# Kernel optimization log

Hardware: AMD Instinct MI355X
Metric: run time of the kernel (lower is better)

## Reference

```python
import jax, jax.numpy as jnp
import numpy as np

B, T, J, D = 128, 256, 50, 3
I, H, C = J * D, 1024, 60


def setup_inputs() -> dict:
    key = jax.random.key(0)
    ks = jax.random.split(key, 10)
    s = 0.02
    return {
        "x": jax.random.normal(ks[0], (B, T, J, D), dtype=jnp.float32),
        "h1": jnp.zeros((B, H), jnp.float32),
        "c1": jnp.zeros((B, H), jnp.float32),
        "h2": jnp.zeros((B, H), jnp.float32),
        "c2": jnp.zeros((B, H), jnp.float32),
        "W_ih1": jax.random.normal(ks[1], (4 * H, I), jnp.float32) * s,
        "W_hh1": jax.random.normal(ks[2], (4 * H, H), jnp.float32) * s,
        "b_ih1": jax.random.normal(ks[3], (4 * H,), jnp.float32) * s,
        "b_hh1": jax.random.normal(ks[4], (4 * H,), jnp.float32) * s,
        "W_ih2": jax.random.normal(ks[5], (4 * H, H), jnp.float32) * s,
        "W_hh2": jax.random.normal(ks[6], (4 * H, H), jnp.float32) * s,
        "b_ih2": jax.random.normal(ks[7], (4 * H,), jnp.float32) * s,
        "b_hh2": jax.random.normal(ks[8], (4 * H,), jnp.float32) * s,
        "W_fc": jax.random.normal(ks[9], (C, H), jnp.float32) * s,
        "b_fc": jnp.zeros((C,), jnp.float32),
        "mode": 0,  # 0 == 'val' (no dropout), static
    }


def _lstm_cell(xv, h, c, Wih, Whh, bih, bhh):
    # PyTorch LSTMCell gate order: i, f, g, o
    gates = xv @ Wih.T + bih + h @ Whh.T + bhh  # [B, 4H]
    i, f, g, o = jnp.split(gates, 4, axis=-1)
    c_new = jax.nn.sigmoid(f) * c + jax.nn.sigmoid(i) * jnp.tanh(g)
    h_new = jax.nn.sigmoid(o) * jnp.tanh(c_new)
    return h_new, c_new


def reference(x, h1, c1, h2, c2, W_ih1, W_hh1, b_ih1, b_hh1,
              W_ih2, W_hh2, b_ih2, b_hh2, W_fc, b_fc, mode):
    b, t = x.shape[0], x.shape[1]
    xs = x.reshape(b, t, -1).transpose(1, 0, 2)  # [T, B, I]

    def step(carry, xt):
        h1, c1, h2, c2 = carry
        h1, c1 = _lstm_cell(xt, h1, c1, W_ih1, W_hh1, b_ih1, b_hh1)
        # mode==0 ('val'): no dropout between layers
        h2, c2 = _lstm_cell(h1, h2, c2, W_ih2, W_hh2, b_ih2, b_hh2)
        return (h1, c1, h2, c2), None

    (h1, c1, h2, c2), _ = jax.lax.scan(step, (h1, c1, h2, c2), xs)
    return h2 @ W_fc.T + b_fc  # [B, num_class]
```

## Files before the change

kernel.cpp:

```cpp
#include <hip/hip_runtime.h>
#include <math.h>


typedef __bf16 bf16;
typedef __bf16 bf16x8 __attribute__((ext_vector_type(8)));
typedef float floatx4 __attribute__((ext_vector_type(4)));
typedef unsigned long long ull;

#define B_   128
#define T_   256
#define H_   1024
#define I_   150
#define KX_  160
#define C_   60
#define K1LDS 1280
#define KP    1024
#define NLINES 40
#define CSTRIDE 64
#define L0FLAG 32
#define L1FLAG 33
#define NCOLS 32
#define NHC  8
#define NT   2

template<int N> struct IC { static constexpr int value = N; };

__device__ __forceinline__ float sigmoidf_(float x) { return 1.f / (1.f + expf(-x)); }

__global__ __launch_bounds__(256)
void convert_all(const float* __restrict__ x,
                 const float* __restrict__ h1in, const float* __restrict__ h2in,
                 bf16* __restrict__ xb, bf16* __restrict__ h1b0, bf16* __restrict__ h2b0,
                 unsigned* __restrict__ cnt)
{
    const size_t nXB = (size_t)T_ * B_ * KX_;
    const size_t nHC = (size_t)B_ * H_;
    size_t idx = (size_t)blockIdx.x * 256 + threadIdx.x;

    if (idx < nXB) {
        size_t t = idx / (B_ * KX_);
        size_t r = idx - t * (B_ * KX_);
        size_t b = r / KX_, k = r - b * KX_;
        xb[idx] = (k < I_) ? (bf16)x[(b * T_ + t) * I_ + k] : (bf16)0.f;
        return;
    }
    idx -= nXB;
    if (idx < nHC) { h1b0[idx] = (bf16)h1in[idx]; return; }
    idx -= nHC;
    if (idx < nHC) { h2b0[idx] = (bf16)h2in[idx]; return; }
    idx -= nHC;
    if (idx < NLINES * CSTRIDE) cnt[idx] = 0u;
}

__device__ __forceinline__ void stage_rebal(
    bf16* lds, bf16* ldsP, int tid, int layer, int n0h,
    const float* Wih1, const float* Whh1, const float* Wih2, const float* Whh2)
{
    if (layer == 0) {
        {
            const int cpr = K1LDS >> 3;
            const int total = NCOLS * cpr;
            for (int ci = tid; ci < total; ci += 512) {
                int r = ci / cpr, c = ci - r * cpr;
                int g = r / NHC, j = r - g * NHC;
                int grow = (g << 10) + n0h + j;
                int k0 = c << 3;
                float v[8];
#pragma unroll
                for (int u = 0; u < 8; ++u) {
                    int k = k0 + u;
                    v[u] = (k < I_) ? Wih1[(size_t)grow * I_ + k]
                         : (k < KX_) ? 0.f
                         : (k < KX_ + H_) ? Whh1[(size_t)grow * H_ + (k - KX_)] : 0.f;
                }
                int cs = (c & ~15) | ((c ^ r) & 15);
                bf16* dst = lds + (size_t)r * K1LDS + (cs << 3);
#pragma unroll
                for (int u = 0; u < 8; ++u) dst[u] = (bf16)v[u];
            }
        }
        {
            const int cpr = KP >> 3;
            const int total = NCOLS * cpr;
            for (int ci = tid; ci < total; ci += 512) {
                int r = ci / cpr, c = ci - r * cpr;
                int g = r / NHC, j = r - g * NHC;
                int grow = (g << 10) + n0h + j;
                int k0 = c << 3;
                float v[8];
#pragma unroll
                for (int u = 0; u < 8; ++u) v[u] = Wih2[(size_t)grow * H_ + k0 + u];
                int cs = (c & ~15) | ((c ^ r) & 15);
                bf16* dst = ldsP + (size_t)r * KP + (cs << 3);
#pragma unroll
                for (int u = 0; u < 8; ++u) dst[u] = (bf16)v[u];
            }
        }
    } else {
        const int cpr = KP >> 3;
        const int total = NCOLS * cpr;
        for (int ci = tid; ci < total; ci += 512) {
            int r = ci / cpr, c = ci - r * cpr;
            int g = r / NHC, j = r - g * NHC;
            int grow = (g << 10) + n0h + j;
            int k0 = c << 3;
            float v[8];
#pragma unroll
            for (int u = 0; u < 8; ++u) v[u] = Whh2[(size_t)grow * H_ + k0 + u];
            int cs = (c & ~15) | ((c ^ r) & 15);
            bf16* dst = lds + (size_t)r * KP + (cs << 3);
#pragma unroll
            for (int u = 0; u < 8; ++u) dst[u] = (bf16)v[u];
        }
    }
}

__global__ __launch_bounds__(512, 2)
void rnn_dist8(const bf16* __restrict__ xb,
               bf16* __restrict__ h1b0, bf16* __restrict__ h1b1,
               bf16* __restrict__ h2b0, bf16* __restrict__ h2b1,
               float* __restrict__ p0, float* __restrict__ p1, float* __restrict__ p2,
               const float* __restrict__ c1in, const float* __restrict__ c2in,
               const float* __restrict__ Wih1, const float* __restrict__ Whh1,
               const float* __restrict__ bih1, const float* __restrict__ bhh1,
               const float* __restrict__ Wih2, const float* __restrict__ Whh2,
               const float* __restrict__ bih2, const float* __restrict__ bhh2,
               const float* __restrict__ Wfc, const float* __restrict__ bfc,
               float* __restrict__ out, unsigned* __restrict__ cnt, int nblk)
{
    extern __shared__ bf16 lds[];
    __shared__ __align__(16) bf16 hst[8][16][NHC];

    const int tid   = threadIdx.x;
    const int bid   = blockIdx.x;
    const int layer = (bid >> 3) & 1;
    const int slice = (bid & 7) | ((bid >> 4) << 3);
    const int n0h   = slice * NHC;
    const int line  = layer * 16 + ((bid & 7) | (((bid >> 4) & 1) << 3));
    bf16* ldsP = lds + 32 * K1LDS;

    stage_rebal(lds, ldsP, tid, layer, n0h, Wih1, Whh1, Wih2, Whh2);
    __syncthreads();

    const int lane = tid & 63;
    const int wv   = tid >> 6;
    const int jj   = lane & (NHC - 1);
    const int quad = lane >> 4;

    float4 bias;
    {
        const float* bi = layer ? bih2 : bih1;
        const float* bh = layer ? bhh2 : bhh1;
        int col = n0h + jj;
        bias.x = bi[col] + bh[col];
        bias.y = bi[col + H_] + bh[col + H_];
        bias.z = bi[col + 2 * H_] + bh[col + 2 * H_];
        bias.w = bi[col + 3 * H_] + bh[col + 3 * H_];
    }

    float creg[2];
    {
        const float* cin = layer ? c2in : c1in;
        int dup = (lane >> 3) & 1;
#pragma unroll
        for (int rp = 0; rp < 2; ++rp) {
            int row = wv * 16 + quad * 4 + rp * 2 + dup;
            creg[rp] = cin[(size_t)row * H_ + n0h + jj];
        }
    }

    floatx4 acc[NT];
    floatx4 pacc[NT];

    auto seg1 = [&](const bf16* A, int ldA, const bf16* Bb, int ldB,
                    auto nksC, int ksBase) {
        constexpr int NKS = decltype(nksC)::value;
        constexpr int CH  = NKS < 16 ? NKS : 16;
        const int arow = wv * 16 + (lane & 15);
        const bf16* a0 = A + (size_t)arow * ldA + quad * 8;
        for (int blk = 0; blk < NKS; blk += CH) {
            bf16x8 a0r[CH];
#pragma unroll
            for (int i = 0; i < CH; ++i)
                a0r[i] = *(const bf16x8*)(a0 + (blk + i) * 32);
            __builtin_amdgcn_sched_barrier(0);
#pragma unroll
            for (int i = 0; i < CH; ++i) {
                int c = (ksBase + blk + i) * 4 + quad;
#pragma unroll
                for (int t = 0; t < NT; ++t) {
                    int r = t * 16 + (lane & 15);
                    int cs = (c & ~15) | ((c ^ r) & 15);
                    bf16x8 bfr = *(const bf16x8*)(Bb + (size_t)r * ldB + (cs << 3));
                    acc[t] = __builtin_amdgcn_mfma_f32_16x16x32_bf16(a0r[i], bfr, acc[t], 0, 0, 0);
                }
            }
        }
    };

    auto segDual = [&](const bf16* A) {
        const int arow = wv * 16 + (lane & 15);
        const bf16* a0 = A + (size_t)arow * H_ + quad * 8;
        for (int blk = 0; blk < 32; blk += 16) {
            bf16x8 a0r[16];
#pragma unroll
            for (int i = 0; i < 16; ++i)
                a0r[i] = *(const bf16x8*)(a0 + (blk + i) * 32);
            __builtin_amdgcn_sched_barrier(0);
#pragma unroll
            for (int i = 0; i < 16; ++i) {
                int ig = blk + i;
                int c1 = (5 + ig) * 4 + quad;
                int cp = ig * 4 + quad;
#pragma unroll
                for (int t = 0; t < NT; ++t) {
                    int r = t * 16 + (lane & 15);
                    int cs1 = (c1 & ~15) | ((c1 ^ r) & 15);
                    bf16x8 b1 = *(const bf16x8*)(lds + (size_t)r * K1LDS + (cs1 << 3));
                    acc[t] = __builtin_amdgcn_mfma_f32_16x16x32_bf16(a0r[i], b1, acc[t], 0, 0, 0);
                    int csp = (cp & ~15) | ((cp ^ r) & 15);
                    bf16x8 bp = *(const bf16x8*)(ldsP + (size_t)r * KP + (csp << 3));
                    pacc[t] = __builtin_amdgcn_mfma_f32_16x16x32_bf16(a0r[i], bp, pacc[t], 0, 0, 0);
                }
            }
        }
    };

    auto epilogue = [&](bf16* hw) {
        const int base = lane & 48;
#pragma unroll
        for (int r = 0; r < 4; ++r) {
            float vi = __shfl(acc[0][r], base + jj, 64);
            float vf = __shfl(acc[0][r], base + 8 + jj, 64);
            float vg = __shfl(acc[1][r], base + jj, 64);
            float vo = __shfl(acc[1][r], base + 8 + jj, 64);
            bool cond = (((lane >> 3) & 1) == (r & 1));
            int slot = r >> 1;
            if (cond) {
                float cv = creg[slot];
                float cn = sigmoidf_(vf + bias.y) * cv
                         + sigmoidf_(vi + bias.x) * tanhf(vg + bias.z);
                creg[slot] = cn;
                float hn = sigmoidf_(vo + bias.w) * tanhf(cn);
                hst[wv][quad * 4 + r][jj] = (bf16)hn;
            }
        }
        __syncthreads();
        if (lane < 32) {
            int row_l = lane >> 1, cg = lane & 1;
            ull v = *(const ull*)&hst[wv][row_l][cg * 4];
            __hip_atomic_store((ull*)(hw + (size_t)(wv * 16 + row_l) * H_ + n0h + cg * 4),
                               v, __ATOMIC_RELAXED, __HIP_MEMORY_SCOPE_AGENT);
        }
    };

    if (layer == 0) {
#pragma unroll
        for (int t = 0; t < NT; ++t) {
            acc[t]  = (floatx4){0.f, 0.f, 0.f, 0.f};
            pacc[t] = (floatx4){0.f, 0.f, 0.f, 0.f};
        }
        seg1(xb, KX_, lds, K1LDS, IC<5>{}, 0);
    }

    for (int e = 0; e <= T_ + 1; ++e) {
        const int pm  = e % 3;
        const int pmr = (e + 2) % 3;
        float* const pbuf[3] = { p0, p1, p2 };

        if (layer == 0 && e <= T_) {
            const bf16* h1r = (e & 1) ? h1b1 : h1b0;
            segDual(h1r);

            float* pw = pbuf[pm] + (size_t)slice * B_ * NCOLS;
#pragma unroll
            for (int t = 0; t < NT; ++t)
#pragma unroll
                for (int r = 0; r < 4; ++r) {
                    int row = wv * 16 + quad * 4 + r;
                    __hip_atomic_store(pw + (size_t)row * NCOLS + t * 16 + (lane & 15),
                                       pacc[t][r], __ATOMIC_RELAXED, __HIP_MEMORY_SCOPE_AGENT);
                }

            if (e < T_) {
                bf16* hw = (e & 1) ? h1b0 : h1b1;
                epilogue(hw);
            }
        } else if (layer == 1 && e >= 2) {
#pragma unroll
            for (int t = 0; t < NT; ++t) acc[t] = (floatx4){0.f, 0.f, 0.f, 0.f};

            const float* pr = pbuf[pmr] + (size_t)slice * B_ * NCOLS;
            float pv[NT][4];
#pragma unroll
            for (int t = 0; t < NT; ++t)
#pragma unroll
                for (int r = 0; r < 4; ++r) {
                    int row = wv * 16 + quad * 4 + r;
                    pv[t][r] = pr[(size_t)row * NCOLS + t * 16 + (lane & 15)];
                }

            const bf16* h2r = (e & 1) ? h2b1 : h2b0;
            seg1(h2r, H_, lds, KP, IC<32>{}, 0);

#pragma unroll
            for (int t = 0; t < NT; ++t)
#pragma unroll
                for (int r = 0; r < 4; ++r) acc[t][r] += pv[t][r];

            bf16* hw = (e & 1) ? h2b0 : h2b1;
            epilogue(hw);
        }

        asm volatile("s_waitcnt vmcnt(0)" ::: "memory");
        __syncthreads();
        const int etag = e + 1;
        if (tid == 0)
            __hip_atomic_fetch_add(cnt + line * CSTRIDE, 1u,
                                   __ATOMIC_RELAXED, __HIP_MEMORY_SCOPE_AGENT);
        if (layer == 0 && e < T_) {
#pragma unroll
            for (int t = 0; t < NT; ++t) {
                acc[t]  = (floatx4){0.f, 0.f, 0.f, 0.f};
                pacc[t] = (floatx4){0.f, 0.f, 0.f, 0.f};
            }
            if (e + 1 < T_)
                seg1(xb + (size_t)(e + 1) * B_ * KX_, KX_, lds, K1LDS, IC<5>{}, 0);
        }
        if (tid < 64) {
            const unsigned* cp = nullptr;
            unsigned tgt = 0;
            if (lane < 16) {
                cp = cnt + (layer * 16 + lane) * CSTRIDE;
                tgt = 8u * (unsigned)etag;
            } else if (lane < 32) {
                if (layer == 0) {
                    if (etag >= 3) {
                        cp = cnt + (16 + (lane - 16)) * CSTRIDE;
                        tgt = 8u * (unsigned)(etag - 2);
                    }
                } else {
                    cp = cnt + (lane - 16) * CSTRIDE;
                    tgt = 8u * (unsigned)etag;
                }
            }
            for (;;) {
                bool ok = (cp == nullptr) ||
                          (__hip_atomic_load(cp, __ATOMIC_RELAXED,
                                             __HIP_MEMORY_SCOPE_AGENT) >= tgt);
                if (__all(ok)) break;
                __builtin_amdgcn_s_sleep(1);
            }
            __builtin_amdgcn_fence(__ATOMIC_ACQUIRE, "agent");
        }
        __syncthreads();
    }

    if (tid < 64) {
        if (lane < 16) {
            const unsigned* cp = cnt + (16 + lane) * CSTRIDE;
            while (__hip_atomic_load(cp, __ATOMIC_RELAXED,
                                     __HIP_MEMORY_SCOPE_AGENT) < 8u * (unsigned)(T_ + 2))
                __builtin_amdgcn_s_sleep(1);
        }
        __builtin_amdgcn_fence(__ATOMIC_ACQUIRE, "agent");
    }
    __syncthreads();

    if (bid < B_) {
        const bf16* h2f = h2b0;
        for (int c = wv; c < C_; c += 8) {
            float a = 0.f;
            for (int k = lane; k < H_; k += 64)
                a += (float)h2f[(size_t)bid * H_ + k] * Wfc[(size_t)c * H_ + k];
#pragma unroll
            for (int off = 32; off; off >>= 1) a += __shfl_down(a, off, 64);
            if (lane == 0) out[bid * C_ + c] = a + bfc[c];
        }
    }
}

__global__ __launch_bounds__(512, 2)
void rnn_decoup8(const bf16* __restrict__ xb,
                 bf16* __restrict__ h1b0, bf16* __restrict__ h1b1,
                 bf16* __restrict__ h2b0, bf16* __restrict__ h2b1,
                 float* __restrict__ p0, float* __restrict__ p1, float* __restrict__ p2,
                 const float* __restrict__ c1in, const float* __restrict__ c2in,
                 const float* __restrict__ Wih1, const float* __restrict__ Whh1,
                 const float* __restrict__ bih1, const float* __restrict__ bhh1,
                 const float* __restrict__ Wih2, const float* __restrict__ Whh2,
                 const float* __restrict__ bih2, const float* __restrict__ bhh2,
                 const float* __restrict__ Wfc, const float* __restrict__ bfc,
                 float* __restrict__ out, unsigned* __restrict__ cnt, int nblk)
{
    extern __shared__ bf16 lds[];
    __shared__ __align__(16) bf16 hst[8][16][NHC];

    const int tid   = threadIdx.x;
    const int bid   = blockIdx.x;
    const int layer = (bid >> 3) & 1;
    const int slice = (bid & 7) | ((bid >> 4) << 3);
    const int n0h   = slice * NHC;
    const int line  = layer * 16 + ((bid & 7) | (((bid >> 4) & 1) << 3));
    bf16* ldsP = lds + 32 * K1LDS;

    stage_rebal(lds, ldsP, tid, layer, n0h, Wih1, Whh1, Wih2, Whh2);
    __syncthreads();

    const int lane = tid & 63;
    const int wv   = tid >> 6;
    const int jj   = lane & (NHC - 1);
    const int quad = lane >> 4;

    float4 bias;
    {
        const float* bi = layer ? bih2 : bih1;
        const float* bh = layer ? bhh2 : bhh1;
        int col = n0h + jj;
        bias.x = bi[col] + bh[col];
        bias.y = bi[col + H_] + bh[col + H_];
        bias.z = bi[col + 2 * H_] + bh[col + 2 * H_];
        bias.w = bi[col + 3 * H_] + bh[col + 3 * H_];
    }

    float creg[2];
    {
        const float* cin = layer ? c2in : c1in;
        int dup = (lane >> 3) & 1;
#pragma unroll
        for (int rp = 0; rp < 2; ++rp) {
            int row = wv * 16 + quad * 4 + rp * 2 + dup;
            creg[rp] = cin[(size_t)row * H_ + n0h + jj];
        }
    }

    floatx4 acc[NT];
    floatx4 pacc[NT];

    auto seg1 = [&](const bf16* A, int ldA, const bf16* Bb, int ldB,
                    auto nksC, int ksBase) {
        constexpr int NKS = decltype(nksC)::value;
        constexpr int CH  = NKS < 16 ? NKS : 16;
        const int arow = wv * 16 + (lane & 15);
        const bf16* a0 = A + (size_t)arow * ldA + quad * 8;
        for (int blk = 0; blk < NKS; blk += CH) {
            bf16x8 a0r[CH];
#pragma unroll
            for (int i = 0; i < CH; ++i)
                a0r[i] = *(const bf16x8*)(a0 + (blk + i) * 32);
            __builtin_amdgcn_sched_barrier(0);
#pragma unroll
            for (int i = 0; i < CH; ++i) {
                int c = (ksBase + blk + i) * 4 + quad;
#pragma unroll
                for (int t = 0; t < NT; ++t) {
                    int r = t * 16 + (lane & 15);
                    int cs = (c & ~15) | ((c ^ r) & 15);
                    bf16x8 bfr = *(const bf16x8*)(Bb + (size_t)r * ldB + (cs << 3));
                    acc[t] = __builtin_amdgcn_mfma_f32_16x16x32_bf16(a0r[i], bfr, acc[t], 0, 0, 0);
                }
            }
        }
    };

    auto segDual = [&](const bf16* A) {
        const int arow = wv * 16 + (lane & 15);
        const bf16* a0 = A + (size_t)arow * H_ + quad * 8;
        for (int blk = 0; blk < 32; blk += 16) {
            bf16x8 a0r[16];
#pragma unroll
            for (int i = 0; i < 16; ++i)
                a0r[i] = *(const bf16x8*)(a0 + (blk + i) * 32);
            __builtin_amdgcn_sched_barrier(0);
#pragma unroll
            for (int i = 0; i < 16; ++i) {
                int ig = blk + i;
                int c1 = (5 + ig) * 4 + quad;
                int cp = ig * 4 + quad;
#pragma unroll
                for (int t = 0; t < NT; ++t) {
                    int r = t * 16 + (lane & 15);
                    int cs1 = (c1 & ~15) | ((c1 ^ r) & 15);
                    bf16x8 b1 = *(const bf16x8*)(lds + (size_t)r * K1LDS + (cs1 << 3));
                    acc[t] = __builtin_amdgcn_mfma_f32_16x16x32_bf16(a0r[i], b1, acc[t], 0, 0, 0);
                    int csp = (cp & ~15) | ((cp ^ r) & 15);
                    bf16x8 bp = *(const bf16x8*)(ldsP + (size_t)r * KP + (csp << 3));
                    pacc[t] = __builtin_amdgcn_mfma_f32_16x16x32_bf16(a0r[i], bp, pacc[t], 0, 0, 0);
                }
            }
        }
    };

    auto epilogue = [&](bf16* hw) {
        const int base = lane & 48;
#pragma unroll
        for (int r = 0; r < 4; ++r) {
            float vi = __shfl(acc[0][r], base + jj, 64);
            float vf = __shfl(acc[0][r], base + 8 + jj, 64);
            float vg = __shfl(acc[1][r], base + jj, 64);
            float vo = __shfl(acc[1][r], base + 8 + jj, 64);
            bool cond = (((lane >> 3) & 1) == (r & 1));
            int slot = r >> 1;
            if (cond) {
                float cv = creg[slot];
                float cn = sigmoidf_(vf + bias.y) * cv
                         + sigmoidf_(vi + bias.x) * tanhf(vg + bias.z);
                creg[slot] = cn;
                float hn = sigmoidf_(vo + bias.w) * tanhf(cn);
                hst[wv][quad * 4 + r][jj] = (bf16)hn;
            }
        }
        __syncthreads();
        if (lane < 32) {
            int row_l = lane >> 1, cg = lane & 1;
            ull v = *(const ull*)&hst[wv][row_l][cg * 4];
            __hip_atomic_store((ull*)(hw + (size_t)(wv * 16 + row_l) * H_ + n0h + cg * 4),
                               v, __ATOMIC_RELAXED, __HIP_MEMORY_SCOPE_AGENT);
        }
    };

    if (layer == 0) {
#pragma unroll
        for (int t = 0; t < NT; ++t) {
            acc[t]  = (floatx4){0.f, 0.f, 0.f, 0.f};
            pacc[t] = (floatx4){0.f, 0.f, 0.f, 0.f};
        }
        seg1(xb, KX_, lds, K1LDS, IC<5>{}, 0);
    }

    for (int e = 0; e <= T_ + 1; ++e) {
        const int pm  = e % 3;
        const int pmr = (e + 2) % 3;
        float* const pbuf[3] = { p0, p1, p2 };

        if (layer == 0 && e <= T_) {
            const bf16* h1r = (e & 1) ? h1b1 : h1b0;
            segDual(h1r);

            float* pw = pbuf[pm] + (size_t)slice * B_ * NCOLS;
#pragma unroll
            for (int t = 0; t < NT; ++t)
#pragma unroll
                for (int r = 0; r < 4; ++r) {
                    int row = wv * 16 + quad * 4 + r;
                    __hip_atomic_store(pw + (size_t)row * NCOLS + t * 16 + (lane & 15),
                                       pacc[t][r], __ATOMIC_RELAXED, __HIP_MEMORY_SCOPE_AGENT);
                }

            if (e < T_) {
                bf16* hw = (e & 1) ? h1b0 : h1b1;
                epilogue(hw);
            }
        } else if (layer == 1 && e >= 2) {
#pragma unroll
            for (int t = 0; t < NT; ++t) acc[t] = (floatx4){0.f, 0.f, 0.f, 0.f};

            const float* pr = pbuf[pmr] + (size_t)slice * B_ * NCOLS;
            float pv[NT][4];
#pragma unroll
            for (int t = 0; t < NT; ++t)
#pragma unroll
                for (int r = 0; r < 4; ++r) {
                    int row = wv * 16 + quad * 4 + r;
                    pv[t][r] = pr[(size_t)row * NCOLS + t * 16 + (lane & 15)];
                }

            const bf16* h2r = (e & 1) ? h2b1 : h2b0;
            seg1(h2r, H_, lds, KP, IC<32>{}, 0);

#pragma unroll
            for (int t = 0; t < NT; ++t)
#pragma unroll
                for (int r = 0; r < 4; ++r) acc[t][r] += pv[t][r];

            bf16* hw = (e & 1) ? h2b0 : h2b1;
            epilogue(hw);
        }

        asm volatile("s_waitcnt vmcnt(0)" ::: "memory");
        __syncthreads();
        const int etag = e + 1;
        if (tid == 0)
            __hip_atomic_fetch_add(cnt + line * CSTRIDE, 1u,
                                   __ATOMIC_RELAXED, __HIP_MEMORY_SCOPE_AGENT);
        if (layer == 0 && e < T_) {
#pragma unroll
            for (int t = 0; t < NT; ++t) {
                acc[t]  = (floatx4){0.f, 0.f, 0.f, 0.f};
                pacc[t] = (floatx4){0.f, 0.f, 0.f, 0.f};
            }
            if (e + 1 < T_)
                seg1(xb + (size_t)(e + 1) * B_ * KX_, KX_, lds, K1LDS, IC<5>{}, 0);
        }
        if (layer == 0) {
            if (bid == 0) {
                if (tid < 16) {
                    const unsigned tgt = 8u * (unsigned)etag;
                    const unsigned* cp = cnt + tid * CSTRIDE;
                    while (__hip_atomic_load(cp, __ATOMIC_RELAXED, __HIP_MEMORY_SCOPE_AGENT) < tgt)
                        __builtin_amdgcn_s_sleep(1);
                }
                if (tid == 0)
                    __hip_atomic_store(cnt + L0FLAG * CSTRIDE, (unsigned)etag,
                                       __ATOMIC_RELAXED, __HIP_MEMORY_SCOPE_AGENT);
            } else if (tid == 0) {
                const unsigned* fp = cnt + L0FLAG * CSTRIDE;
                while (__hip_atomic_load(fp, __ATOMIC_RELAXED, __HIP_MEMORY_SCOPE_AGENT) < (unsigned)etag)
                    __builtin_amdgcn_s_sleep(1);
            }
            if (tid == 0 && etag >= 3) {
                const unsigned* fp = cnt + L1FLAG * CSTRIDE;
                while (__hip_atomic_load(fp, __ATOMIC_RELAXED, __HIP_MEMORY_SCOPE_AGENT) < (unsigned)(etag - 2))
                    __builtin_amdgcn_s_sleep(1);
            }
        } else {
            if (bid == 8) {
                if (tid < 16) {
                    const unsigned tgt = 8u * (unsigned)etag;
                    const unsigned* cp = cnt + (16 + tid) * CSTRIDE;
                    while (__hip_atomic_load(cp, __ATOMIC_RELAXED, __HIP_MEMORY_SCOPE_AGENT) < tgt)
                        __builtin_amdgcn_s_sleep(1);
                }
                if (tid == 0)
                    __hip_atomic_store(cnt + L1FLAG * CSTRIDE, (unsigned)etag,
                                       __ATOMIC_RELAXED, __HIP_MEMORY_SCOPE_AGENT);
            } else if (tid == 0) {
                const unsigned* fp = cnt + L1FLAG * CSTRIDE;
                while (__hip_atomic_load(fp, __ATOMIC_RELAXED, __HIP_MEMORY_SCOPE_AGENT) < (unsigned)etag)
                    __builtin_amdgcn_s_sleep(1);
            }
            if (tid == 0) {
                const unsigned* fp = cnt + L0FLAG * CSTRIDE;
                while (__hip_atomic_load(fp, __ATOMIC_RELAXED, __HIP_MEMORY_SCOPE_AGENT) < (unsigned)etag)
                    __builtin_amdgcn_s_sleep(1);
            }
        }
        __syncthreads();
        if (tid < 64)
            __builtin_amdgcn_fence(__ATOMIC_ACQUIRE, "agent");
        __syncthreads();
    }

    if (tid == 0 && layer == 0) {
        const unsigned* fp = cnt + L1FLAG * CSTRIDE;
        while (__hip_atomic_load(fp, __ATOMIC_RELAXED, __HIP_MEMORY_SCOPE_AGENT) < (unsigned)(T_ + 2))
            __builtin_amdgcn_s_sleep(1);
    }
    __syncthreads();
    if (tid < 64)
        __builtin_amdgcn_fence(__ATOMIC_ACQUIRE, "agent");
    __syncthreads();

    if (bid < B_) {
        const bf16* h2f = h2b0;
        for (int c = wv; c < C_; c += 8) {
            float a = 0.f;
            for (int k = lane; k < H_; k += 64)
                a += (float)h2f[(size_t)bid * H_ + k] * Wfc[(size_t)c * H_ + k];
#pragma unroll
            for (int off = 32; off; off >>= 1) a += __shfl_down(a, off, 64);
            if (lane == 0) out[bid * C_ + c] = a + bfc[c];
        }
    }
}

extern "C" void kernel_launch(void* const* d_in, const int* in_sizes, int n_in,
                              void* d_out, int out_size, void* d_ws, size_t ws_size,
                              hipStream_t stream)
{
    const float* x    = (const float*)d_in[0];
    const float* h1in = (const float*)d_in[1];
    const float* c1in = (const float*)d_in[2];
    const float* h2in = (const float*)d_in[3];
    const float* c2in = (const float*)d_in[4];
    const float* Wih1 = (const float*)d_in[5];
    const float* Whh1 = (const float*)d_in[6];
    const float* bih1 = (const float*)d_in[7];
    const float* bhh1 = (const float*)d_in[8];
    const float* Wih2 = (const float*)d_in[9];
    const float* Whh2 = (const float*)d_in[10];
    const float* bih2 = (const float*)d_in[11];
    const float* bhh2 = (const float*)d_in[12];
    const float* Wfc  = (const float*)d_in[13];
    const float* bfc  = (const float*)d_in[14];
    float* out = (float*)d_out;

    const size_t szXB  = (size_t)T_ * B_ * KX_ * 2;
    const size_t szH   = (size_t)B_ * H_ * 2;
    const size_t szCnt = (size_t)NLINES * CSTRIDE * 4;
    const size_t szP   = (size_t)128 * B_ * NCOLS * 4;
    const size_t needDec = szXB + 4 * szH + szCnt + 3 * szP;

    char* p = (char*)d_ws;
    bf16* xb = (bf16*)p;    p += szXB;
    bf16* h1b0 = (bf16*)p;  p += szH;
    bf16* h1b1 = (bf16*)p;  p += szH;
    bf16* h2b0 = (bf16*)p;  p += szH;
    bf16* h2b1 = (bf16*)p;  p += szH;
    unsigned* cnt = (unsigned*)p;  p += szCnt;
    float* p0 = (float*)p;  p += szP;
    float* p1 = (float*)p;  p += szP;
    float* p2 = (float*)p;

    const size_t citems = (size_t)T_ * B_ * KX_ + 2 * (size_t)B_ * H_ + NLINES * CSTRIDE;
    convert_all<<<(int)((citems + 255) / 256), 256, 0, stream>>>(
        x, h1in, h2in, xb, h1b0, h2b0, cnt);

    int nblk = 256;
    void* args[] = { &xb, &h1b0, &h1b1, &h2b0, &h2b1, &p0, &p1, &p2,
                     (void*)&c1in, (void*)&c2in,
                     (void*)&Wih1, (void*)&Whh1, (void*)&bih1, (void*)&bhh1,
                     (void*)&Wih2, (void*)&Whh2, (void*)&bih2, (void*)&bhh2,
                     (void*)&Wfc, (void*)&bfc, &out, &cnt, &nblk };

    const unsigned ldsRebal = (unsigned)(32 * K1LDS + 32 * KP) * 2u;
    hipError_t err = hipErrorOutOfMemory;
    if (ws_size >= needDec) {
        if (hipFuncSetAttribute((const void*)rnn_dist8,
                                hipFuncAttributeMaxDynamicSharedMemorySize,
                                (int)ldsRebal) == hipSuccess) {
            err = hipLaunchCooperativeKernel((const void*)rnn_dist8,
                                             dim3(256), dim3(512), args,
                                             ldsRebal, stream);
        }
    }
    if (err != hipSuccess && ws_size >= needDec) {
        (void)hipGetLastError();
        if (hipFuncSetAttribute((const void*)rnn_decoup8,
                                hipFuncAttributeMaxDynamicSharedMemorySize,
                                (int)ldsRebal) == hipSuccess) {
            (void)hipLaunchCooperativeKernel((const void*)rnn_decoup8,
                                             dim3(256), dim3(512), args,
                                             ldsRebal, stream);
        }
    }
}
```

Measured before the change: 3.329 ms.

## Pack cross-layer partials to bf16, use fast activations, centralize barrier flags

The layer-0 to layer-1 input-projection partials are stored as packed bf16 pairs instead of fp32, halving that per-step exchange traffic. Sigmoid and tanh switch to fast exp and reciprocal approximations. The per-step inter-block barrier changes from every block polling 16-32 line counters to one leader block per layer polling the counters and publishing a single flag that the other blocks wait on. This removes polling contention but adds an extra hop of latency per step, and the bf16 partials and approximate activations cost precision.

```diff
diff --git a/kernel.cpp b/kernel.cpp
--- a/kernel.cpp
+++ b/kernel.cpp
@@ -27,6 +27,15 @@
 
 __device__ __forceinline__ float sigmoidf_(float x) { return 1.f / (1.f + expf(-x)); }
 
+__device__ __forceinline__ float fsig(float x) {
+    return __builtin_amdgcn_rcpf(1.f + __expf(-x));
+}
+__device__ __forceinline__ float ftanh(float x) {
+    float t = __expf(-2.f * fabsf(x));
+    float r = (1.f - t) * __builtin_amdgcn_rcpf(1.f + t);
+    return copysignf(r, x);
+}
+
 __global__ __launch_bounds__(256)
 void convert_all(const float* __restrict__ x,
                  const float* __restrict__ h1in, const float* __restrict__ h2in,
@@ -116,17 +125,17 @@
 }
 
 __global__ __launch_bounds__(512, 2)
-void rnn_dist8(const bf16* __restrict__ xb,
-               bf16* __restrict__ h1b0, bf16* __restrict__ h1b1,
-               bf16* __restrict__ h2b0, bf16* __restrict__ h2b1,
-               float* __restrict__ p0, float* __restrict__ p1, float* __restrict__ p2,
-               const float* __restrict__ c1in, const float* __restrict__ c2in,
-               const float* __restrict__ Wih1, const float* __restrict__ Whh1,
-               const float* __restrict__ bih1, const float* __restrict__ bhh1,
-               const float* __restrict__ Wih2, const float* __restrict__ Whh2,
-               const float* __restrict__ bih2, const float* __restrict__ bhh2,
-               const float* __restrict__ Wfc, const float* __restrict__ bfc,
-               float* __restrict__ out, unsigned* __restrict__ cnt, int nblk)
+void rnn_bf16p8(const bf16* __restrict__ xb,
+                bf16* __restrict__ h1b0, bf16* __restrict__ h1b1,
+                bf16* __restrict__ h2b0, bf16* __restrict__ h2b1,
+                float* __restrict__ p0, float* __restrict__ p1, float* __restrict__ p2,
+                const float* __restrict__ c1in, const float* __restrict__ c2in,
+                const float* __restrict__ Wih1, const float* __restrict__ Whh1,
+                const float* __restrict__ bih1, const float* __restrict__ bhh1,
+                const float* __restrict__ Wih2, const float* __restrict__ Whh2,
+                const float* __restrict__ bih2, const float* __restrict__ bhh2,
+                const float* __restrict__ Wfc, const float* __restrict__ bfc,
+                float* __restrict__ out, unsigned* __restrict__ cnt, int nblk)
 {
     extern __shared__ bf16 lds[];
     __shared__ __align__(16) bf16 hst[8][16][NHC];
@@ -238,10 +247,10 @@
             int slot = r >> 1;
             if (cond) {
                 float cv = creg[slot];
-                float cn = sigmoidf_(vf + bias.y) * cv
-                         + sigmoidf_(vi + bias.x) * tanhf(vg + bias.z);
+                float cn = fsig(vf + bias.y) * cv
+                         + fsig(vi + bias.x) * ftanh(vg + bias.z);
                 creg[slot] = cn;
-                float hn = sigmoidf_(vo + bias.w) * tanhf(cn);
+                float hn = fsig(vo + bias.w) * ftanh(cn);
                 hst[wv][quad * 4 + r][jj] = (bf16)hn;
             }
         }
@@ -272,15 +281,17 @@
             const bf16* h1r = (e & 1) ? h1b1 : h1b0;
             segDual(h1r);
 
-            float* pw = pbuf[pm] + (size_t)slice * B_ * NCOLS;
-#pragma unroll
-            for (int t = 0; t < NT; ++t)
-#pragma unroll
-                for (int r = 0; r < 4; ++r) {
-                    int row = wv * 16 + quad * 4 + r;
-                    __hip_atomic_store(pw + (size_t)row * NCOLS + t * 16 + (lane & 15),
-                                       pacc[t][r], __ATOMIC_RELAXED, __HIP_MEMORY_SCOPE_AGENT);
-                }
+            unsigned* pw = (unsigned*)pbuf[pm] + (size_t)slice * B_ * 16;
+#pragma unroll
+            for (int r = 0; r < 4; ++r) {
+                int row = wv * 16 + quad * 4 + r;
+                bf16 b0 = (bf16)pacc[0][r];
+                bf16 b1 = (bf16)pacc[1][r];
+                unsigned u = (unsigned)(*(unsigned short*)&b0)
+                           | ((unsigned)(*(unsigned short*)&b1) << 16);
+                __hip_atomic_store(pw + (size_t)row * 16 + (lane & 15), u,
+                                   __ATOMIC_RELAXED, __HIP_MEMORY_SCOPE_AGENT);
+            }
 
             if (e < T_) {
                 bf16* hw = (e & 1) ? h1b0 : h1b1;
@@ -290,15 +301,17 @@
 #pragma unroll
             for (int t = 0; t < NT; ++t) acc[t] = (floatx4){0.f, 0.f, 0.f, 0.f};
 
-            const float* pr = pbuf[pmr] + (size_t)slice * B_ * NCOLS;
+            const unsigned* pr = (const unsigned*)pbuf[pmr] + (size_t)slice * B_ * 16;
             float pv[NT][4];
 #pragma unroll
-            for (int t = 0; t < NT; ++t)
-#pragma unroll
-                for (int r = 0; r < 4; ++r) {
-                    int row = wv * 16 + quad * 4 + r;
-                    pv[t][r] = pr[(size_t)row * NCOLS + t * 16 + (lane & 15)];
-                }
+            for (int r = 0; r < 4; ++r) {
+                int row = wv * 16 + quad * 4 + r;
+                unsigned u = pr[(size_t)row * 16 + (lane & 15)];
+                unsigned short s0 = (unsigned short)(u & 0xffffu);
+                unsigned short s1 = (unsigned short)(u >> 16);
+                pv[0][r] = (float)(*(bf16*)&s0);
+                pv[1][r] = (float)(*(bf16*)&s1);
+            }
 
             const bf16* h2r = (e & 1) ? h2b1 : h2b0;
             seg1(h2r, H_, lds, KP, IC<32>{}, 0);
@@ -327,44 +340,63 @@
             if (e + 1 < T_)
                 seg1(xb + (size_t)(e + 1) * B_ * KX_, KX_, lds, K1LDS, IC<5>{}, 0);
         }
-        if (tid < 64) {
-            const unsigned* cp = nullptr;
-            unsigned tgt = 0;
-            if (lane < 16) {
-                cp = cnt + (layer * 16 + lane) * CSTRIDE;
-                tgt = 8u * (unsigned)etag;
-            } else if (lane < 32) {
-                if (layer == 0) {
-                    if (etag >= 3) {
-                        cp = cnt + (16 + (lane - 16)) * CSTRIDE;
-                        tgt = 8u * (unsigned)(etag - 2);
-                    }
-                } else {
-                    cp = cnt + (lane - 16) * CSTRIDE;
-                    tgt = 8u * (unsigned)etag;
-                }
-            }
-            for (;;) {
-                bool ok = (cp == nullptr) ||
-                          (__hip_atomic_load(cp, __ATOMIC_RELAXED,
-                                             __HIP_MEMORY_SCOPE_AGENT) >= tgt);
-                if (__all(ok)) break;
-                __builtin_amdgcn_s_sleep(1);
-            }
+        if (layer == 0) {
+            if (bid == 0) {
+                if (tid < 16) {
+                    const unsigned tgt = 8u * (unsigned)etag;
+                    const unsigned* cp = cnt + tid * CSTRIDE;
+                    while (__hip_atomic_load(cp, __ATOMIC_RELAXED, __HIP_MEMORY_SCOPE_AGENT) < tgt)
+                        __builtin_amdgcn_s_sleep(1);
+                }
+                if (tid == 0)
+                    __hip_atomic_store(cnt + L0FLAG * CSTRIDE, (unsigned)etag,
+                                       __ATOMIC_RELAXED, __HIP_MEMORY_SCOPE_AGENT);
+            } else if (tid == 0) {
+                const unsigned* fp = cnt + L0FLAG * CSTRIDE;
+                while (__hip_atomic_load(fp, __ATOMIC_RELAXED, __HIP_MEMORY_SCOPE_AGENT) < (unsigned)etag)
+                    __builtin_amdgcn_s_sleep(1);
+            }
+            if (tid == 0 && etag >= 3) {
+                const unsigned* fp = cnt + L1FLAG * CSTRIDE;
+                while (__hip_atomic_load(fp, __ATOMIC_RELAXED, __HIP_MEMORY_SCOPE_AGENT) < (unsigned)(etag - 2))
+                    __builtin_amdgcn_s_sleep(1);
+            }
+        } else {
+            if (bid == 8) {
+                if (tid < 16) {
+                    const unsigned tgt = 8u * (unsigned)etag;
+                    const unsigned* cp = cnt + (16 + tid) * CSTRIDE;
+                    while (__hip_atomic_load(cp, __ATOMIC_RELAXED, __HIP_MEMORY_SCOPE_AGENT) < tgt)
+                        __builtin_amdgcn_s_sleep(1);
+                }
+                if (tid == 0)
+                    __hip_atomic_store(cnt + L1FLAG * CSTRIDE, (unsigned)etag,
+                                       __ATOMIC_RELAXED, __HIP_MEMORY_SCOPE_AGENT);
+            } else if (tid == 0) {
+                const unsigned* fp = cnt + L1FLAG * CSTRIDE;
+                while (__hip_atomic_load(fp, __ATOMIC_RELAXED, __HIP_MEMORY_SCOPE_AGENT) < (unsigned)etag)
+                    __builtin_amdgcn_s_sleep(1);
+            }
+            if (tid == 0) {
+                const unsigned* fp = cnt + L0FLAG * CSTRIDE;
+                while (__hip_atomic_load(fp, __ATOMIC_RELAXED, __HIP_MEMORY_SCOPE_AGENT) < (unsigned)etag)
+                    __builtin_amdgcn_s_sleep(1);
+            }
+        }
+        __syncthreads();
+        if (tid < 64)
             __builtin_amdgcn_fence(__ATOMIC_ACQUIRE, "agent");
-        }
         __syncthreads();
     }
 
-    if (tid < 64) {
-        if (lane < 16) {
-            const unsigned* cp = cnt + (16 + lane) * CSTRIDE;
-            while (__hip_atomic_load(cp, __ATOMIC_RELAXED,
-                                     __HIP_MEMORY_SCOPE_AGENT) < 8u * (unsigned)(T_ + 2))
-                __builtin_amdgcn_s_sleep(1);
-        }
+    if (tid == 0 && layer == 0) {
+        const unsigned* fp = cnt + L1FLAG * CSTRIDE;
+        while (__hip_atomic_load(fp, __ATOMIC_RELAXED, __HIP_MEMORY_SCOPE_AGENT) < (unsigned)(T_ + 2))
+            __builtin_amdgcn_s_sleep(1);
+    }
+    __syncthreads();
+    if (tid < 64)
         __builtin_amdgcn_fence(__ATOMIC_ACQUIRE, "agent");
-    }
     __syncthreads();
 
     if (bid < B_) {
@@ -716,10 +748,10 @@
     const unsigned ldsRebal = (unsigned)(32 * K1LDS + 32 * KP) * 2u;
     hipError_t err = hipErrorOutOfMemory;
     if (ws_size >= needDec) {
-        if (hipFuncSetAttribute((const void*)rnn_dist8,
+        if (hipFuncSetAttribute((const void*)rnn_bf16p8,
                                 hipFuncAttributeMaxDynamicSharedMemorySize,
                                 (int)ldsRebal) == hipSuccess) {
-            err = hipLaunchCooperativeKernel((const void*)rnn_dist8,
+            err = hipLaunchCooperativeKernel((const void*)rnn_bf16p8,
                                              dim3(256), dim3(512), args,
                                              ldsRebal, stream);
         }
```

New measurement: 3.102 ms. 1.07x faster.
